# Kernel tuning notes

Hardware: AMD Instinct MI355X
Metric: run time of the kernel (lower is better)

The kernel has to match this reference:

```python
import jax, jax.numpy as jnp
import numpy as np

TEMP = 1.0

def _mlp(x, W1, b1, W2, b2):
    # Linear -> ReLU -> Linear ('cnt' head: no final activation, no bn/skip)
    h = jax.nn.relu(jnp.einsum('bmd,dh->bmh', x, W1) + b1)
    return jnp.einsum('bmh,hk->bmk', h, W2) + b2


def setup_inputs() -> dict:
    key = jax.random.key(0)
    ks = jax.random.split(key, 9)
    B, M, D, H, K = 16, 2048, 128, 256, 64
    s1 = 1.0 / np.sqrt(D)
    s2 = 1.0 / np.sqrt(H)
    return {
        'x':   jax.random.normal(ks[0], (B, M, D), dtype=jnp.float32),
        'qW1': jax.random.normal(ks[1], (D, H), dtype=jnp.float32) * s1,
        'qb1': jnp.zeros((H,), dtype=jnp.float32),
        'qW2': jax.random.normal(ks[2], (H, K), dtype=jnp.float32) * s2,
        'qb2': jnp.zeros((K,), dtype=jnp.float32),
        'kW1': jax.random.normal(ks[3], (D, H), dtype=jnp.float32) * s1,
        'kb1': jnp.zeros((H,), dtype=jnp.float32),
        'kW2': jax.random.normal(ks[4], (H, K), dtype=jnp.float32) * s2,
        'kb2': jnp.zeros((K,), dtype=jnp.float32),
    }


def reference(x, qW1, qb1, qW2, qb2, kW1, kb1, kW2, kb2):
    queries = _mlp(x, qW1, qb1, qW2, qb2)   # [B, M, K]
    keys    = _mlp(x, kW1, kb1, kW2, kb2)   # [B, M, K]
    qkt = jnp.einsum('bik,bjk->bij', queries, keys)          # [B, M, M]
    row_max = jnp.max(qkt, axis=-1, keepdims=True)           # [B, M, 1]
    dist = jax.nn.softmax(TEMP * qkt / row_max, axis=-1)     # max-DIVISION normalization (not subtraction)
    return dist
```

## Files before the change

kernel.cpp:

```cpp
#include <hip/hip_runtime.h>

#define B_   16
#define M_   2048
#define D_   128
#define H_   256
#define K_   64
#define ROWS (B_ * M_)

typedef short short8 __attribute__((ext_vector_type(8)));
typedef short short4v __attribute__((ext_vector_type(4)));
typedef float f32x4  __attribute__((ext_vector_type(4)));

static constexpr size_t OFF_QHI = 0;
static constexpr size_t OFF_QLO = (size_t)ROWS * K_;
static constexpr size_t OFF_KHI = 2 * (size_t)ROWS * K_;
static constexpr size_t OFF_W1H = 3 * (size_t)ROWS * K_;
static constexpr size_t OFF_W1L = OFF_W1H + 2 * (size_t)D_ * H_;
static constexpr size_t OFF_W2H = OFF_W1L + 2 * (size_t)D_ * H_;
static constexpr size_t OFF_W2L = OFF_W2H + 2 * (size_t)H_ * K_;

static __device__ __forceinline__ float bf2f(short u) {
    union { unsigned int u; float f; } c;
    c.u = ((unsigned int)(unsigned short)u) << 16;
    return c.f;
}
static __device__ __forceinline__ short f2bf(float f) {
    union { float f; unsigned int u; } c; c.f = f;
    unsigned int u = c.u + 0x7fffu + ((c.u >> 16) & 1u);
    return (short)(u >> 16);
}
static __device__ __forceinline__ void split2(float v, short& hi, short& lo) {
    hi = f2bf(v);
    lo = f2bf(v - bf2f(hi));
}
static __device__ __forceinline__ f32x4 mfma16(short8 a, short8 b, f32x4 c) {
    return __builtin_amdgcn_mfma_f32_16x16x32_bf16(a, b, c, 0, 0, 0);
}

__global__ __launch_bounds__(256) void prep_w(
    const float* __restrict__ qW1, const float* __restrict__ kW1,
    const float* __restrict__ qW2, const float* __restrict__ kW2,
    short* __restrict__ ws)
{
    const int which = blockIdx.y;
    const float* src; short* dhi; short* dlo; int N, Kd;
    if (which == 0)      { src = qW1; dhi = ws + OFF_W1H;            dlo = ws + OFF_W1L;            N = H_; Kd = D_; }
    else if (which == 1) { src = kW1; dhi = ws + OFF_W1H + D_ * H_;  dlo = ws + OFF_W1L + D_ * H_;  N = H_; Kd = D_; }
    else if (which == 2) { src = qW2; dhi = ws + OFF_W2H;            dlo = ws + OFF_W2L;            N = K_; Kd = H_; }
    else                 { src = kW2; dhi = ws + OFF_W2H + H_ * K_;  dlo = ws + OFF_W2L + H_ * K_;  N = K_; Kd = H_; }
    int idx = blockIdx.x * 256 + threadIdx.x;
    if (idx < N * Kd) {
        int n = idx / Kd, k = idx % Kd;
        float v = src[(size_t)k * N + n];
        short hi, lo; split2(v, hi, lo);
        dhi[idx] = hi; dlo[idx] = lo;
    }
}

__global__ __launch_bounds__(128) void mlp_kernel(
    const float* __restrict__ x,
    short* __restrict__ ws,
    const float* __restrict__ qb1, const float* __restrict__ kb1,
    const float* __restrict__ qb2, const float* __restrict__ kb2)
{
    const int head = blockIdx.y;
    const short* W1H = ws + OFF_W1H + (size_t)head * (D_ * H_);
    const short* W1L = ws + OFF_W1L + (size_t)head * (D_ * H_);
    const short* W2H = ws + OFF_W2H + (size_t)head * (H_ * K_);
    const short* W2L = ws + OFF_W2L + (size_t)head * (H_ * K_);
    const float* b1  = head ? kb1 : qb1;
    const float* b2  = head ? kb2 : qb2;
    short* ohi       = ws + (head ? OFF_KHI : OFF_QHI);
    short* olo       = ws + OFF_QLO;

    const int tid  = threadIdx.x;
    const int w    = tid >> 6;
    const int lane = tid & 63;
    const int l15  = lane & 15;
    const int quad = lane >> 4;
    const int r0   = (blockIdx.x * 2 + w) * 16;

    __shared__ __align__(16) short hsh[2][16][264];
    __shared__ __align__(16) short hsl[2][16][264];

    short8 ah[4], al[4];
    const float* xrow = x + (size_t)(r0 + l15) * D_ + quad * 8;
    #pragma unroll
    for (int ks = 0; ks < 4; ++ks) {
        float4 v0 = *(const float4*)(xrow + ks * 32);
        float4 v1 = *(const float4*)(xrow + ks * 32 + 4);
        float vv[8] = {v0.x, v0.y, v0.z, v0.w, v1.x, v1.y, v1.z, v1.w};
        #pragma unroll
        for (int j = 0; j < 8; ++j) {
            short hi, lo; split2(vv[j], hi, lo);
            ah[ks][j] = hi; al[ks][j] = lo;
        }
    }

    #pragma unroll
    for (int jt = 0; jt < 16; ++jt) {
        f32x4 acc = {0.f, 0.f, 0.f, 0.f};
        const size_t wro = (size_t)(jt * 16 + l15) * D_ + quad * 8;
        #pragma unroll
        for (int ks = 0; ks < 4; ++ks) {
            short8 bh = *(const short8*)(W1H + wro + ks * 32);
            short8 bl = *(const short8*)(W1L + wro + ks * 32);
            acc = mfma16(bh, ah[ks], acc);
            acc = mfma16(bh, al[ks], acc);
            acc = mfma16(bl, ah[ks], acc);
        }
        float4 bias4 = *(const float4*)(b1 + jt * 16 + quad * 4);
        short4v hi4, lo4;
        #pragma unroll
        for (int r = 0; r < 4; ++r) {
            float v = acc[r] + ((const float*)&bias4)[r];
            v = v > 0.f ? v : 0.f;
            short hi, lo; split2(v, hi, lo);
            hi4[r] = hi; lo4[r] = lo;
        }
        *(short4v*)&hsh[w][l15][jt * 16 + quad * 4] = hi4;
        *(short4v*)&hsl[w][l15][jt * 16 + quad * 4] = lo4;
    }

    short8 gh[8], gl[8];
    #pragma unroll
    for (int ks = 0; ks < 8; ++ks) {
        gh[ks] = *(const short8*)&hsh[w][l15][ks * 32 + quad * 8];
        gl[ks] = *(const short8*)&hsl[w][l15][ks * 32 + quad * 8];
    }
    #pragma unroll
    for (int jt = 0; jt < 4; ++jt) {
        f32x4 acc = {0.f, 0.f, 0.f, 0.f};
        const size_t wro = (size_t)(jt * 16 + l15) * H_ + quad * 8;
        #pragma unroll
        for (int ks = 0; ks < 8; ++ks) {
            short8 bh = *(const short8*)(W2H + wro + ks * 32);
            short8 bl = *(const short8*)(W2L + wro + ks * 32);
            acc = mfma16(bh, gh[ks], acc);
            acc = mfma16(bh, gl[ks], acc);
            acc = mfma16(bl, gh[ks], acc);
        }
        float4 bias4 = *(const float4*)(b2 + jt * 16 + quad * 4);
        const size_t oi = (size_t)(r0 + l15) * K_ + jt * 16 + quad * 4;
        if (head == 0) {
            short4v hi4, lo4;
            #pragma unroll
            for (int r = 0; r < 4; ++r) {
                float v = acc[r] + ((const float*)&bias4)[r];
                short hi, lo; split2(v, hi, lo);
                hi4[r] = hi; lo4[r] = lo;
            }
            *(short4v*)(ohi + oi) = hi4;
            *(short4v*)(olo + oi) = lo4;
        } else {
            short4v hi4;
            #pragma unroll
            for (int r = 0; r < 4; ++r)
                hi4[r] = f2bf(acc[r] + ((const float*)&bias4)[r]);
            *(short4v*)(ohi + oi) = hi4;
        }
    }
}

__global__ __launch_bounds__(512, 4) void scores_kernel(
    const short* __restrict__ ws,
    float* __restrict__ out)
{
    const int flat = blockIdx.x;
    const int xcd  = flat & 7;
    const int slot = flat >> 3;
    const int bb   = (slot & 1) * 8 + xcd;
    const int i0   = (slot >> 1) * 16;
    const int tid  = threadIdx.x;
    const int w    = tid >> 6;
    const int lane = tid & 63;
    const int l15  = lane & 15;
    const int quad = lane >> 4;

    const short* Qh = ws + OFF_QHI + (size_t)bb * M_ * K_;
    const short* Ql = ws + OFF_QLO + (size_t)bb * M_ * K_;
    const short* Kh = ws + OFF_KHI + (size_t)bb * M_ * K_;

    const size_t qo = (size_t)(i0 + l15) * K_ + quad * 8;
    short8 qh0 = *(const short8*)(Qh + qo);
    short8 qh1 = *(const short8*)(Qh + qo + 32);
    short8 ql0 = *(const short8*)(Ql + qo);
    short8 ql1 = *(const short8*)(Ql + qo + 32);

    f32x4 s[16];
    #pragma unroll
    for (int t = 0; t < 16; ++t) {
        const int j0 = (w * 16 + t) * 16;
        const size_t ko = (size_t)(j0 + l15) * K_ + quad * 8;
        short8 kh0 = *(const short8*)(Kh + ko);
        short8 kh1 = *(const short8*)(Kh + ko + 32);
        f32x4 acc = {0.f, 0.f, 0.f, 0.f};
        acc = mfma16(kh0, qh0, acc);
        acc = mfma16(kh0, ql0, acc);
        acc = mfma16(kh1, qh1, acc);
        acc = mfma16(kh1, ql1, acc);
        s[t] = acc;
    }

    f32x4 vmx = s[0], vmn = s[0];
    #pragma unroll
    for (int t = 1; t < 16; ++t)
        #pragma unroll
        for (int r = 0; r < 4; ++r) {
            vmx[r] = fmaxf(vmx[r], s[t][r]);
            vmn[r] = fminf(vmn[r], s[t][r]);
        }
    float mx = fmaxf(fmaxf(vmx[0], vmx[1]), fmaxf(vmx[2], vmx[3]));
    float mn = fminf(fminf(vmn[0], vmn[1]), fminf(vmn[2], vmn[3]));
    mx = fmaxf(mx, __shfl_xor(mx, 16));  mn = fminf(mn, __shfl_xor(mn, 16));
    mx = fmaxf(mx, __shfl_xor(mx, 32));  mn = fminf(mn, __shfl_xor(mn, 32));

    __shared__ float redmax[8][16], redmin[8][16], redsum[8][16];
    if (lane < 16) { redmax[w][l15] = mx; redmin[w][l15] = mn; }
    __syncthreads();

    float mm = redmax[0][l15], nn = redmin[0][l15];
    #pragma unroll
    for (int ww = 1; ww < 8; ++ww) {
        mm = fmaxf(mm, redmax[ww][l15]);
        nn = fminf(nn, redmin[ww][l15]);
    }
    const float inv = 1.0f / mm;
    const float nz  = -fmaxf(1.0f, nn * inv);

    float lsum = 0.f;
    #pragma unroll
    for (int t = 0; t < 16; ++t)
        #pragma unroll
        for (int r = 0; r < 4; ++r) {
            float e = __expf(fmaf(s[t][r], inv, nz));
            s[t][r] = e;
            lsum += e;
        }
    lsum += __shfl_xor(lsum, 16);
    lsum += __shfl_xor(lsum, 32);
    if (lane < 16) redsum[w][l15] = lsum;
    __syncthreads();

    float tot = 0.f;
    #pragma unroll
    for (int ww = 0; ww < 8; ++ww) tot += redsum[ww][l15];
    const float invsum = 1.0f / tot;

    float* ob = out + (size_t)bb * M_ * M_ + (size_t)(i0 + l15) * M_;
    #pragma unroll
    for (int t = 0; t < 16; ++t) {
        f32x4 v;
        #pragma unroll
        for (int r = 0; r < 4; ++r) v[r] = s[t][r] * invsum;
        __builtin_nontemporal_store(v, (f32x4*)(ob + (w * 16 + t) * 16 + quad * 4));
    }
}

extern "C" void kernel_launch(void* const* d_in, const int* in_sizes, int n_in,
                              void* d_out, int out_size, void* d_ws, size_t ws_size,
                              hipStream_t stream)
{
    (void)in_sizes; (void)n_in; (void)out_size; (void)ws_size;
    const float* x   = (const float*)d_in[0];
    const float* qW1 = (const float*)d_in[1];
    const float* qb1 = (const float*)d_in[2];
    const float* qW2 = (const float*)d_in[3];
    const float* qb2 = (const float*)d_in[4];
    const float* kW1 = (const float*)d_in[5];
    const float* kb1 = (const float*)d_in[6];
    const float* kW2 = (const float*)d_in[7];
    const float* kb2 = (const float*)d_in[8];
    short* ws  = (short*)d_ws;
    float* out = (float*)d_out;

    prep_w<<<dim3(128, 4), 256, 0, stream>>>(qW1, kW1, qW2, kW2, ws);
    mlp_kernel<<<dim3(ROWS / 32, 2), 128, 0, stream>>>(x, ws, qb1, kb1, qb2, kb2);
    scores_kernel<<<dim3(2048), 512, 0, stream>>>(ws, out);
}
```

Measured before the change: 464.2 us.

## Process two row tiles per wave in MLP kernel and chunk hidden dimension

Each wave of the MLP kernel now handles 32 rows (two 16-row tiles), so every W1/W2 fragment loaded from global memory feeds two sets of MFMAs. The hidden dimension is split into two 128-wide phases, and the second GEMM accumulates across phases, which halves the LDS staging buffer. The grid is halved to match. This raises register pressure (two x-fragment sets plus eight output accumulators), and fewer blocks may reduce occupancy. The MLP kernel is likely a small share of total time next to the scores kernel.

```diff
diff --git a/kernel.cpp b/kernel.cpp
--- a/kernel.cpp
+++ b/kernel.cpp
@@ -78,86 +78,120 @@
     const int lane = tid & 63;
     const int l15  = lane & 15;
     const int quad = lane >> 4;
-    const int r0   = (blockIdx.x * 2 + w) * 16;
-
-    __shared__ __align__(16) short hsh[2][16][264];
-    __shared__ __align__(16) short hsl[2][16][264];
-
-    short8 ah[4], al[4];
-    const float* xrow = x + (size_t)(r0 + l15) * D_ + quad * 8;
-    #pragma unroll
-    for (int ks = 0; ks < 4; ++ks) {
-        float4 v0 = *(const float4*)(xrow + ks * 32);
-        float4 v1 = *(const float4*)(xrow + ks * 32 + 4);
-        float vv[8] = {v0.x, v0.y, v0.z, v0.w, v1.x, v1.y, v1.z, v1.w};
+    const int r0   = (blockIdx.x * 2 + w) * 32;
+
+    __shared__ __align__(16) short hsh[2][2][16][136];
+    __shared__ __align__(16) short hsl[2][2][16][136];
+
+    short8 ah[2][4], al[2][4];
+    #pragma unroll
+    for (int t = 0; t < 2; ++t) {
+        const float* xrow = x + (size_t)(r0 + t * 16 + l15) * D_ + quad * 8;
+        #pragma unroll
+        for (int ks = 0; ks < 4; ++ks) {
+            float4 v0 = *(const float4*)(xrow + ks * 32);
+            float4 v1 = *(const float4*)(xrow + ks * 32 + 4);
+            float vv[8] = {v0.x, v0.y, v0.z, v0.w, v1.x, v1.y, v1.z, v1.w};
+            #pragma unroll
+            for (int j = 0; j < 8; ++j) {
+                short hi, lo; split2(vv[j], hi, lo);
+                ah[t][ks][j] = hi; al[t][ks][j] = lo;
+            }
+        }
+    }
+
+    f32x4 acc2[2][4];
+    #pragma unroll
+    for (int t = 0; t < 2; ++t)
+        #pragma unroll
+        for (int j = 0; j < 4; ++j)
+            acc2[t][j] = f32x4{0.f, 0.f, 0.f, 0.f};
+
+    #pragma unroll
+    for (int ph = 0; ph < 2; ++ph) {
         #pragma unroll
         for (int j = 0; j < 8; ++j) {
-            short hi, lo; split2(vv[j], hi, lo);
-            ah[ks][j] = hi; al[ks][j] = lo;
-        }
-    }
-
-    #pragma unroll
-    for (int jt = 0; jt < 16; ++jt) {
-        f32x4 acc = {0.f, 0.f, 0.f, 0.f};
-        const size_t wro = (size_t)(jt * 16 + l15) * D_ + quad * 8;
-        #pragma unroll
-        for (int ks = 0; ks < 4; ++ks) {
-            short8 bh = *(const short8*)(W1H + wro + ks * 32);
-            short8 bl = *(const short8*)(W1L + wro + ks * 32);
-            acc = mfma16(bh, ah[ks], acc);
-            acc = mfma16(bh, al[ks], acc);
-            acc = mfma16(bl, ah[ks], acc);
-        }
-        float4 bias4 = *(const float4*)(b1 + jt * 16 + quad * 4);
-        short4v hi4, lo4;
-        #pragma unroll
-        for (int r = 0; r < 4; ++r) {
-            float v = acc[r] + ((const float*)&bias4)[r];
-            v = v > 0.f ? v : 0.f;
-            short hi, lo; split2(v, hi, lo);
-            hi4[r] = hi; lo4[r] = lo;
-        }
-        *(short4v*)&hsh[w][l15][jt * 16 + quad * 4] = hi4;
-        *(short4v*)&hsl[w][l15][jt * 16 + quad * 4] = lo4;
-    }
-
-    short8 gh[8], gl[8];
-    #pragma unroll
-    for (int ks = 0; ks < 8; ++ks) {
-        gh[ks] = *(const short8*)&hsh[w][l15][ks * 32 + quad * 8];
-        gl[ks] = *(const short8*)&hsl[w][l15][ks * 32 + quad * 8];
-    }
-    #pragma unroll
-    for (int jt = 0; jt < 4; ++jt) {
-        f32x4 acc = {0.f, 0.f, 0.f, 0.f};
-        const size_t wro = (size_t)(jt * 16 + l15) * H_ + quad * 8;
-        #pragma unroll
-        for (int ks = 0; ks < 8; ++ks) {
-            short8 bh = *(const short8*)(W2H + wro + ks * 32);
-            short8 bl = *(const short8*)(W2L + wro + ks * 32);
-            acc = mfma16(bh, gh[ks], acc);
-            acc = mfma16(bh, gl[ks], acc);
-            acc = mfma16(bl, gh[ks], acc);
-        }
-        float4 bias4 = *(const float4*)(b2 + jt * 16 + quad * 4);
-        const size_t oi = (size_t)(r0 + l15) * K_ + jt * 16 + quad * 4;
-        if (head == 0) {
-            short4v hi4, lo4;
+            const int jt = ph * 8 + j;
+            f32x4 a0 = {0.f, 0.f, 0.f, 0.f};
+            f32x4 a1 = {0.f, 0.f, 0.f, 0.f};
+            const size_t wro = (size_t)(jt * 16 + l15) * D_ + quad * 8;
+            #pragma unroll
+            for (int ks = 0; ks < 4; ++ks) {
+                short8 bh = *(const short8*)(W1H + wro + ks * 32);
+                short8 bl = *(const short8*)(W1L + wro + ks * 32);
+                a0 = mfma16(bh, ah[0][ks], a0);
+                a0 = mfma16(bh, al[0][ks], a0);
+                a0 = mfma16(bl, ah[0][ks], a0);
+                a1 = mfma16(bh, ah[1][ks], a1);
+                a1 = mfma16(bh, al[1][ks], a1);
+                a1 = mfma16(bl, ah[1][ks], a1);
+            }
+            float4 bias4 = *(const float4*)(b1 + jt * 16 + quad * 4);
+            short4v h4, l4;
             #pragma unroll
             for (int r = 0; r < 4; ++r) {
-                float v = acc[r] + ((const float*)&bias4)[r];
+                float v = a0[r] + ((const float*)&bias4)[r];
+                v = v > 0.f ? v : 0.f;
                 short hi, lo; split2(v, hi, lo);
-                hi4[r] = hi; lo4[r] = lo;
-            }
-            *(short4v*)(ohi + oi) = hi4;
-            *(short4v*)(olo + oi) = lo4;
-        } else {
-            short4v hi4;
-            #pragma unroll
-            for (int r = 0; r < 4; ++r)
-                hi4[r] = f2bf(acc[r] + ((const float*)&bias4)[r]);
-            *(short4v*)(ohi + oi) = hi4;
+                h4[r] = hi; l4[r] = lo;
+            }
+            *(short4v*)&hsh[w][0][l15][j * 16 + quad * 4] = h4;
+            *(short4v*)&hsl[w][0][l15][j * 16 + quad * 4] = l4;
+            #pragma unroll
+            for (int r = 0; r < 4; ++r) {
+                float v = a1[r] + ((const float*)&bias4)[r];
+                v = v > 0.f ? v : 0.f;
+                short hi, lo; split2(v, hi, lo);
+                h4[r] = hi; l4[r] = lo;
+            }
+            *(short4v*)&hsh[w][1][l15][j * 16 + quad * 4] = h4;
+            *(short4v*)&hsl[w][1][l15][j * 16 + quad * 4] = l4;
+        }
+
+        #pragma unroll
+        for (int kk = 0; kk < 4; ++kk) {
+            short8 g0h = *(const short8*)&hsh[w][0][l15][kk * 32 + quad * 8];
+            short8 g0l = *(const short8*)&hsl[w][0][l15][kk * 32 + quad * 8];
+            short8 g1h = *(const short8*)&hsh[w][1][l15][kk * 32 + quad * 8];
+            short8 g1l = *(const short8*)&hsl[w][1][l15][kk * 32 + quad * 8];
+            #pragma unroll
+            for (int jt2 = 0; jt2 < 4; ++jt2) {
+                const size_t wro2 = (size_t)(jt2 * 16 + l15) * H_ + ph * 128 + kk * 32 + quad * 8;
+                short8 bh = *(const short8*)(W2H + wro2);
+                short8 bl = *(const short8*)(W2L + wro2);
+                acc2[0][jt2] = mfma16(bh, g0h, acc2[0][jt2]);
+                acc2[0][jt2] = mfma16(bh, g0l, acc2[0][jt2]);
+                acc2[0][jt2] = mfma16(bl, g0h, acc2[0][jt2]);
+                acc2[1][jt2] = mfma16(bh, g1h, acc2[1][jt2]);
+                acc2[1][jt2] = mfma16(bh, g1l, acc2[1][jt2]);
+                acc2[1][jt2] = mfma16(bl, g1h, acc2[1][jt2]);
+            }
+        }
+    }
+
+    #pragma unroll
+    for (int jt2 = 0; jt2 < 4; ++jt2) {
+        float4 bias4 = *(const float4*)(b2 + jt2 * 16 + quad * 4);
+        #pragma unroll
+        for (int t = 0; t < 2; ++t) {
+            const size_t oi = (size_t)(r0 + t * 16 + l15) * K_ + jt2 * 16 + quad * 4;
+            if (head == 0) {
+                short4v hi4, lo4;
+                #pragma unroll
+                for (int r = 0; r < 4; ++r) {
+                    float v = acc2[t][jt2][r] + ((const float*)&bias4)[r];
+                    short hi, lo; split2(v, hi, lo);
+                    hi4[r] = hi; lo4[r] = lo;
+                }
+                *(short4v*)(ohi + oi) = hi4;
+                *(short4v*)(olo + oi) = lo4;
+            } else {
+                short4v hi4;
+                #pragma unroll
+                for (int r = 0; r < 4; ++r)
+                    hi4[r] = f2bf(acc2[t][jt2][r] + ((const float*)&bias4)[r]);
+                *(short4v*)(ohi + oi) = hi4;
+            }
         }
     }
 }
@@ -275,6 +309,6 @@
     float* out = (float*)d_out;
 
     prep_w<<<dim3(128, 4), 256, 0, stream>>>(qW1, kW1, qW2, kW2, ws);
-    mlp_kernel<<<dim3(ROWS / 32, 2), 128, 0, stream>>>(x, ws, qb1, kb1, qb2, kb2);
+    mlp_kernel<<<dim3(ROWS / 64, 2), 128, 0, stream>>>(x, ws, qb1, kb1, qb2, kb2);
     scores_kernel<<<dim3(2048), 512, 0, stream>>>(ws, out);
 }
```

New measurement: 415.0 us. 10.6% less time.

## Stage MLP weights in LDS and keep hidden activations in registers

Applied to the files above, without the earlier changes.

The MLP kernel now uses 512-thread blocks of 8 waves covering 128 rows, and stages half of W1 and W2 (hi/lo bf16 splits) into swizzled shared memory per phase. The previous version had every wave read weights straight from global memory. The first-layer output tiles are permuted so the ReLU results land directly in the register layout the second MFMA needs, which removes the LDS round trip for hidden activations. This cuts repeated global and L2 weight traffic but adds barriers and about 100KB of LDS per block, which limits occupancy. The MLP kernel is likely a small share of total time next to the scores kernel.

```diff
diff --git a/kernel.cpp b/kernel.cpp
--- a/kernel.cpp
+++ b/kernel.cpp
@@ -57,7 +57,7 @@
     }
 }
 
-__global__ __launch_bounds__(128) void mlp_kernel(
+__global__ __launch_bounds__(512, 2) void mlp_kernel(
     const float* __restrict__ x,
     short* __restrict__ ws,
     const float* __restrict__ qb1, const float* __restrict__ kb1,
@@ -78,75 +78,108 @@
     const int lane = tid & 63;
     const int l15  = lane & 15;
     const int quad = lane >> 4;
-    const int r0   = (blockIdx.x * 2 + w) * 16;
-
-    __shared__ __align__(16) short hsh[2][16][264];
-    __shared__ __align__(16) short hsl[2][16][264];
+    const int r0   = blockIdx.x * 128 + w * 16;
+
+    __shared__ __align__(16) short w1h_s[128 * 136];
+    __shared__ __align__(16) short w1l_s[128 * 136];
+    __shared__ __align__(16) short w2h_s[64 * 136];
+    __shared__ __align__(16) short w2l_s[64 * 136];
 
     short8 ah[4], al[4];
-    const float* xrow = x + (size_t)(r0 + l15) * D_ + quad * 8;
-    #pragma unroll
-    for (int ks = 0; ks < 4; ++ks) {
-        float4 v0 = *(const float4*)(xrow + ks * 32);
-        float4 v1 = *(const float4*)(xrow + ks * 32 + 4);
-        float vv[8] = {v0.x, v0.y, v0.z, v0.w, v1.x, v1.y, v1.z, v1.w};
-        #pragma unroll
-        for (int j = 0; j < 8; ++j) {
-            short hi, lo; split2(vv[j], hi, lo);
-            ah[ks][j] = hi; al[ks][j] = lo;
-        }
-    }
-
-    #pragma unroll
-    for (int jt = 0; jt < 16; ++jt) {
-        f32x4 acc = {0.f, 0.f, 0.f, 0.f};
-        const size_t wro = (size_t)(jt * 16 + l15) * D_ + quad * 8;
+    {
+        const float* xrow = x + (size_t)(r0 + l15) * D_ + quad * 8;
         #pragma unroll
         for (int ks = 0; ks < 4; ++ks) {
-            short8 bh = *(const short8*)(W1H + wro + ks * 32);
-            short8 bl = *(const short8*)(W1L + wro + ks * 32);
-            acc = mfma16(bh, ah[ks], acc);
-            acc = mfma16(bh, al[ks], acc);
-            acc = mfma16(bl, ah[ks], acc);
-        }
-        float4 bias4 = *(const float4*)(b1 + jt * 16 + quad * 4);
-        short4v hi4, lo4;
-        #pragma unroll
-        for (int r = 0; r < 4; ++r) {
-            float v = acc[r] + ((const float*)&bias4)[r];
-            v = v > 0.f ? v : 0.f;
-            short hi, lo; split2(v, hi, lo);
-            hi4[r] = hi; lo4[r] = lo;
-        }
-        *(short4v*)&hsh[w][l15][jt * 16 + quad * 4] = hi4;
-        *(short4v*)&hsl[w][l15][jt * 16 + quad * 4] = lo4;
-    }
-
-    short8 gh[8], gl[8];
-    #pragma unroll
-    for (int ks = 0; ks < 8; ++ks) {
-        gh[ks] = *(const short8*)&hsh[w][l15][ks * 32 + quad * 8];
-        gl[ks] = *(const short8*)&hsl[w][l15][ks * 32 + quad * 8];
-    }
-    #pragma unroll
-    for (int jt = 0; jt < 4; ++jt) {
-        f32x4 acc = {0.f, 0.f, 0.f, 0.f};
-        const size_t wro = (size_t)(jt * 16 + l15) * H_ + quad * 8;
-        #pragma unroll
-        for (int ks = 0; ks < 8; ++ks) {
-            short8 bh = *(const short8*)(W2H + wro + ks * 32);
-            short8 bl = *(const short8*)(W2L + wro + ks * 32);
-            acc = mfma16(bh, gh[ks], acc);
-            acc = mfma16(bh, gl[ks], acc);
-            acc = mfma16(bl, gh[ks], acc);
-        }
-        float4 bias4 = *(const float4*)(b2 + jt * 16 + quad * 4);
-        const size_t oi = (size_t)(r0 + l15) * K_ + jt * 16 + quad * 4;
+            float4 v0 = *(const float4*)(xrow + ks * 32);
+            float4 v1 = *(const float4*)(xrow + ks * 32 + 4);
+            float vv[8] = {v0.x, v0.y, v0.z, v0.w, v1.x, v1.y, v1.z, v1.w};
+            #pragma unroll
+            for (int j = 0; j < 8; ++j) {
+                short hi, lo; split2(vv[j], hi, lo);
+                ah[ks][j] = hi; al[ks][j] = lo;
+            }
+        }
+    }
+
+    f32x4 acc2[4];
+    #pragma unroll
+    for (int j = 0; j < 4; ++j) acc2[j] = f32x4{0.f, 0.f, 0.f, 0.f};
+
+    #pragma unroll
+    for (int ph = 0; ph < 2; ++ph) {
+        if (ph) __syncthreads();
+
+        #pragma unroll
+        for (int k = 0; k < 4; ++k) {
+            int chunk = tid + k * 512;
+            int row = chunk >> 4, ci = chunk & 15;
+            int cisw = ci ^ (((row >> 3) & 1) << 2);
+            const size_t so = (size_t)(ph * 128 + row) * D_ + ci * 8;
+            *(short8*)&w1h_s[row * 136 + cisw * 8] = *(const short8*)(W1H + so);
+            *(short8*)&w1l_s[row * 136 + cisw * 8] = *(const short8*)(W1L + so);
+        }
+        #pragma unroll
+        for (int k = 0; k < 2; ++k) {
+            int chunk = tid + k * 512;
+            int row = chunk >> 4, ci = chunk & 15;
+            const size_t so = (size_t)row * H_ + ph * 128 + ci * 8;
+            *(short8*)&w2h_s[row * 136 + ci * 8] = *(const short8*)(W2H + so);
+            *(short8*)&w2l_s[row * 136 + ci * 8] = *(const short8*)(W2L + so);
+        }
+        __syncthreads();
+
+        short8 gh[4], gl[4];
+        #pragma unroll
+        for (int jt = 0; jt < 8; ++jt) {
+            const int kk   = jt & 3;
+            const int half = jt >> 2;
+            const int rp   = (kk << 5) + ((l15 >> 2) << 3) + (half << 2) + (l15 & 3);
+            const int sw   = (rp >> 3) & 1;
+            const int base = rp * 136 + quad * 8;
+            f32x4 a0 = {0.f, 0.f, 0.f, 0.f};
+            #pragma unroll
+            for (int ks = 0; ks < 4; ++ks) {
+                const int a = base + (ks ^ sw) * 32;
+                short8 bh = *(const short8*)&w1h_s[a];
+                short8 bl = *(const short8*)&w1l_s[a];
+                a0 = mfma16(bh, ah[ks], a0);
+                a0 = mfma16(bh, al[ks], a0);
+                a0 = mfma16(bl, ah[ks], a0);
+            }
+            float4 bias4 = *(const float4*)(b1 + ph * 128 + kk * 32 + quad * 8 + half * 4);
+            #pragma unroll
+            for (int r = 0; r < 4; ++r) {
+                float v = a0[r] + ((const float*)&bias4)[r];
+                v = v > 0.f ? v : 0.f;
+                short hi, lo; split2(v, hi, lo);
+                gh[kk][half * 4 + r] = hi;
+                gl[kk][half * 4 + r] = lo;
+            }
+        }
+
+        #pragma unroll
+        for (int kk = 0; kk < 4; ++kk) {
+            #pragma unroll
+            for (int jt2 = 0; jt2 < 4; ++jt2) {
+                const int a = (jt2 * 16 + l15) * 136 + kk * 32 + quad * 8;
+                short8 bh = *(const short8*)&w2h_s[a];
+                short8 bl = *(const short8*)&w2l_s[a];
+                acc2[jt2] = mfma16(bh, gh[kk], acc2[jt2]);
+                acc2[jt2] = mfma16(bh, gl[kk], acc2[jt2]);
+                acc2[jt2] = mfma16(bl, gh[kk], acc2[jt2]);
+            }
+        }
+    }
+
+    #pragma unroll
+    for (int jt2 = 0; jt2 < 4; ++jt2) {
+        float4 bias4 = *(const float4*)(b2 + jt2 * 16 + quad * 4);
+        const size_t oi = (size_t)(r0 + l15) * K_ + jt2 * 16 + quad * 4;
         if (head == 0) {
             short4v hi4, lo4;
             #pragma unroll
             for (int r = 0; r < 4; ++r) {
-                float v = acc[r] + ((const float*)&bias4)[r];
+                float v = acc2[jt2][r] + ((const float*)&bias4)[r];
                 short hi, lo; split2(v, hi, lo);
                 hi4[r] = hi; lo4[r] = lo;
             }
@@ -156,7 +189,7 @@
             short4v hi4;
             #pragma unroll
             for (int r = 0; r < 4; ++r)
-                hi4[r] = f2bf(acc[r] + ((const float*)&bias4)[r]);
+                hi4[r] = f2bf(acc2[jt2][r] + ((const float*)&bias4)[r]);
             *(short4v*)(ohi + oi) = hi4;
         }
     }
@@ -275,6 +308,6 @@
     float* out = (float*)d_out;
 
     prep_w<<<dim3(128, 4), 256, 0, stream>>>(qW1, kW1, qW2, kW2, ws);
-    mlp_kernel<<<dim3(ROWS / 32, 2), 128, 0, stream>>>(x, ws, qb1, kb1, qb2, kb2);
+    mlp_kernel<<<dim3(ROWS / 128, 2), 512, 0, stream>>>(x, ws, qb1, kb1, qb2, kb2);
     scores_kernel<<<dim3(2048), 512, 0, stream>>>(ws, out);
 }
```

Result: faster. 396.3 us (-14.6%).
